# Kernel tuning notes

Hardware: AMD Instinct MI355X
Metric: run time of the kernel (lower is better)

Reference implementation:

```python
import jax, jax.numpy as jnp
import numpy as np

B, N, H, FD = 2, 512, 128, 5
NT, SD, L = 3, 4, 3
COPY = 10.0
EPS = 1e-6


def setup_inputs() -> dict:
    key = jax.random.key(0)
    ks = jax.random.split(key, 20)
    node_type = jax.random.randint(ks[0], (B, N, 1), 0, NT).astype(jnp.float32)
    node_state = jax.random.normal(ks[1], (B, N, SD), jnp.float32)
    node_feats = jnp.concatenate([node_type, node_state], axis=-1)  # [B,N,5]
    adj = jax.random.bernoulli(ks[2], 0.05, (B, N, N)).astype(jnp.float32)
    adj = jnp.maximum(adj, adj.transpose(0, 2, 1)) * (1.0 - jnp.eye(N, dtype=jnp.float32))
    scope_node_mask = jax.random.bernoulli(ks[3], 0.5, (B, N)).astype(jnp.float32)
    scope_edge_mask = jax.random.bernoulli(ks[4], 0.5, (B, N, N)).astype(jnp.float32)
    s = 0.02
    p = dict(
        node_feats=node_feats, adj=adj,
        scope_node_mask=scope_node_mask, scope_edge_mask=scope_edge_mask,
        W_in=jax.random.normal(ks[5], (FD, H)) * s, b_in=jnp.zeros((H,)),
        W_mp=jax.random.normal(ks[6], (L, 2 * H, H)) * s, b_mp=jnp.zeros((L, H)),
        Wt1=jax.random.normal(ks[7], (H, H)) * s, bt1=jnp.zeros((H,)),
        Wt2=jax.random.normal(ks[8], (H, NT)) * s, bt2=jnp.zeros((NT,)),
        Ws1=jax.random.normal(ks[9], (H, H)) * s, bs1=jnp.zeros((H,)),
        Ws2=jax.random.normal(ks[10], (H, SD)) * s, bs2=jnp.zeros((SD,)),
        We1=jax.random.normal(ks[11], (4 * H, H)) * s, be1=jnp.zeros((H,)),
        We2=jax.random.normal(ks[12], (H, 3)) * s, be2=jnp.zeros((3,)),
    )
    return p


def _decode_edge_logits(adj, edl, eye):
    probs = jax.nn.softmax(edl, axis=-1)
    p_keep = probs[..., 0]  # EDGE_DELTA_KEEP = 0
    p_add = probs[..., 1]   # EDGE_DELTA_ADD = 1
    cur = (adj > 0.5).astype(edl.dtype)
    p_next = jnp.clip(p_add + p_keep * cur, EPS, 1.0 - EPS)
    el = jnp.log(p_next) - jnp.log1p(-p_next)  # logit
    return jnp.where(eye[None], -1e9, el)


def _forward(node_feats, adj, scope_node_mask, scope_edge_mask,
             W_in, b_in, W_mp, b_mp, Wt1, bt1, Wt2, bt2,
             Ws1, bs1, Ws2, bs2, We1, be1, We2, be2):
    # encoder: input proj + L rounds of [h, adj@h] -> Linear -> ReLU
    h = jax.nn.relu(node_feats @ W_in + b_in)  # [B,N,H]
    for l in range(L):
        msg = jnp.einsum('bij,bjh->bih', adj, h)
        h = jax.nn.relu(jnp.concatenate([h, msg], axis=-1) @ W_mp[l] + b_mp[l])
    # node heads (2-layer MLPs)
    type_local = jax.nn.relu(h @ Wt1 + bt1) @ Wt2 + bt2      # [B,N,NT]
    state_local = jax.nn.relu(h @ Ws1 + bs1) @ Ws2 + bs2     # [B,N,SD]
    # pairwise edge-delta head
    h_i = h[:, :, None, :]
    h_j = h[:, None, :, :]
    pair = jnp.concatenate([
        jnp.broadcast_to(h_i, (B, N, N, H)),
        jnp.broadcast_to(h_j, (B, N, N, H)),
        jnp.abs(h_i - h_j),
        h_i * h_j,
    ], axis=-1)  # [B,N,N,4H]
    edl = jax.nn.relu(pair @ We1 + be1) @ We2 + be2  # [B,N,N,3]
    edl = 0.5 * (edl + edl.transpose(0, 2, 1, 3))
    eye = jnp.eye(N, dtype=bool)
    edl = jnp.where(eye[None, :, :, None], 0.0, edl)
    # merges with copy paths
    cur_type = jnp.clip(node_feats[..., 0].astype(jnp.int32), 0, NT - 1)
    copy_type = jnp.where(jnp.arange(NT) == cur_type[..., None], COPY, -COPY)
    type_full = jnp.where(scope_node_mask[..., None] != 0, type_local, copy_type)
    scope = scope_node_mask[..., None]
    state_full = scope * state_local + (1.0 - scope) * node_feats[..., 1:]
    copy_edl = jnp.broadcast_to(jnp.where(jnp.arange(3) == 0, COPY, -COPY), (B, N, N, 3))
    copy_edl = jnp.where(eye[None, :, :, None], 0.0, copy_edl)
    edl_full = jnp.where(scope_edge_mask[..., None] != 0, edl, copy_edl)
    el_full = _decode_edge_logits(adj, edl_full, eye)
    return type_full, state_full, edl_full, el_full


def reference(node_feats, adj, scope_node_mask, scope_edge_mask,
              W_in, b_in, W_mp, b_mp, Wt1, bt1, Wt2, bt2,
              Ws1, bs1, Ws2, bs2, We1, be1, We2, be2):
    return _forward(node_feats, adj, scope_node_mask, scope_edge_mask,
                    W_in, b_in, W_mp, b_mp, Wt1, bt1, Wt2, bt2,
                    Ws1, bs1, Ws2, bs2, We1, be1, We2, be2)
```

## Files before the change

### kernel.cpp

```cpp
#include <hip/hip_runtime.h>
#include <math.h>

#define B_ 2
#define N_ 512
#define H_ 128
#define NT_ 3
#define SD_ 4
#define FD_ 5

typedef float f32x4 __attribute__((ext_vector_type(4)));
typedef unsigned int u32x4 __attribute__((ext_vector_type(4)));

#define MFMA16(acc, a, b) \
    asm("s_nop 1\n\tv_mfma_f32_16x16x32_bf16 %0, %1, %2, %0" \
        : "+v"(acc) : "v"(a), "v"(b))

#define CVTPK(d, a, b) \
    asm("v_cvt_pk_bf16_f32 %0, %1, %2" : "=v"(d) : "v"(a), "v"(b))

#define CVTPKA(d, a, b) \
    asm("v_cvt_pk_bf16_f32 %0, |%1|, |%2|" : "=v"(d) : "v"(a), "v"(b))

static __device__ inline unsigned rne1(float f) {
    unsigned u = __float_as_uint(f);
    u += 0x7fffu + ((u >> 16) & 1u);
    return u >> 16;
}

__global__ __launch_bounds__(128) void k_input(const float* __restrict__ feats,
                                               const float* __restrict__ W_in,
                                               const float* __restrict__ b_in,
                                               float* __restrict__ hout,
                                               const float* __restrict__ We1,
                                               const float* __restrict__ We2,
                                               unsigned short* __restrict__ wfrag,
                                               unsigned short* __restrict__ wfrag2) {
    int blk = blockIdx.x, tid = threadIdx.x;
    if (blk < B_ * N_) {
        const float* f = feats + (size_t)blk * FD_;
        float acc = b_in[tid];
#pragma unroll
        for (int k = 0; k < FD_; ++k) acc += f[k] * W_in[k * H_ + tid];
        hout[(size_t)blk * H_ + tid] = fmaxf(acc, 0.f);
        return;
    }
    if (blk < B_ * N_ + 32) {
        int t = (blk - B_ * N_) * 128 + tid;
        int lane = t & 63, cg = (t >> 6) & 7, kb = t >> 9;
        int lr = lane & 15, g = lane >> 4;
        int c = cg * 16 + lr;
        unsigned o[4];
#pragma unroll
        for (int p = 0; p < 4; ++p) {
            float a = We1[(size_t)(256 + kb * 32 + 8 * g + 2 * p) * H_ + c];
            float bq = We1[(size_t)(256 + kb * 32 + 8 * g + 2 * p + 1) * H_ + c];
            o[p] = rne1(a) | (rne1(bq) << 16);
        }
        u32x4 v = {o[0], o[1], o[2], o[3]};
        *(u32x4*)(wfrag + (size_t)t * 8) = v;
        return;
    }
    {
        int t = (blk - (B_ * N_ + 32)) * 128 + tid;
        if (t < 256) {
            int kb = t >> 6, lane = t & 63;
            int oc = lane & 15, g = lane >> 4;
            unsigned w[4];
#pragma unroll
            for (int p = 0; p < 4; ++p) {
                int k0 = kb * 32 + g * 8 + 2 * p;
                int k1 = k0 + 1;
                int c0 = ((k0 >> 6) << 6) | ((k0 & 3) << 4) | ((k0 & 63) >> 2);
                int c1 = ((k1 >> 6) << 6) | ((k1 & 3) << 4) | ((k1 & 63) >> 2);
                float v0 = (oc < 3) ? We2[c0 * 3 + oc] : 0.f;
                float v1 = (oc < 3) ? We2[c1 * 3 + oc] : 0.f;
                w[p] = rne1(v0) | (rne1(v1) << 16);
            }
            u32x4 v = {w[0], w[1], w[2], w[3]};
            *(u32x4*)(wfrag2 + (size_t)t * 8) = v;
        }
    }
}

__global__ __launch_bounds__(128) void k_mp(const float* __restrict__ hin,
                                            float* __restrict__ hout,
                                            const float* __restrict__ adj,
                                            const float* __restrict__ Wl,
                                            const float* __restrict__ bl) {
    __shared__ float hi[H_];
    __shared__ float msg[H_];
    __shared__ unsigned short idxs[N_];
    __shared__ float avals[N_];
    __shared__ int cnt2[2];
    int node = blockIdx.x;
    int b = node >> 9;
    int tid = threadIdx.x;
    int w = tid >> 6, lane = tid & 63;
    hi[tid] = hin[(size_t)node * H_ + tid];
    const float* arow = adj + (size_t)node * N_;
    float4 av = ((const float4*)arow)[tid];
    int segbase = w * 256;
    int cum = 0;
#pragma unroll
    for (int q = 0; q < 4; ++q) {
        float a = (&av.x)[q];
        bool pred = (a != 0.f);
        unsigned long long mask = __ballot(pred);
        if (pred) {
            int pos = segbase + cum +
                      (int)__popcll(mask & ((1ull << lane) - 1ull));
            idxs[pos] = (unsigned short)(tid * 4 + q);
            avals[pos] = a;
        }
        cum += (int)__popcll(mask);
    }
    if (lane == 0) cnt2[w] = cum;
    __syncthreads();

    float m = 0.f;
    const float* hb = hin + ((size_t)b * N_) * H_;
    int n0 = cnt2[0], n1 = cnt2[1];
    for (int t = 0; t < n0; ++t)
        m += avals[t] * hb[(size_t)idxs[t] * H_ + tid];
    for (int t = 0; t < n1; ++t)
        m += avals[256 + t] * hb[(size_t)idxs[256 + t] * H_ + tid];
    msg[tid] = m;
    __syncthreads();

    float acc = bl[tid];
#pragma unroll 4
    for (int k = 0; k < H_; ++k) {
        acc += hi[k]  * Wl[(size_t)k * H_ + tid];
        acc += msg[k] * Wl[(size_t)(k + H_) * H_ + tid];
    }
    hout[(size_t)node * H_ + tid] = fmaxf(acc, 0.f);
}

__global__ __launch_bounds__(128) void k_heads(
    const float* __restrict__ h, const float* __restrict__ feats,
    const float* __restrict__ snm,
    const float* __restrict__ Wt1, const float* __restrict__ bt1,
    const float* __restrict__ Wt2, const float* __restrict__ bt2,
    const float* __restrict__ Ws1, const float* __restrict__ bs1,
    const float* __restrict__ Ws2, const float* __restrict__ bs2,
    const float* __restrict__ We1, const float* __restrict__ be1,
    float* __restrict__ Acoef, float* __restrict__ Bcoef,
    unsigned short* __restrict__ hbf,
    float* __restrict__ type_out, float* __restrict__ state_out) {
    __shared__ float hi[H_], hT[H_], hS[H_];
    int node = blockIdx.x, tid = threadIdx.x;
    float hv0 = h[(size_t)node * H_ + tid];
    hi[tid] = hv0;
    hbf[(size_t)node * H_ + tid] = (unsigned short)rne1(hv0);
    __syncthreads();
    float at = bt1[tid], as = bs1[tid], aa = be1[tid], ab = 0.f;
#pragma unroll 4
    for (int k = 0; k < H_; ++k) {
        float hv = hi[k];
        at += hv * Wt1[k * H_ + tid];
        as += hv * Ws1[k * H_ + tid];
        aa += hv * We1[k * H_ + tid];
        ab += hv * We1[(k + H_) * H_ + tid];
    }
    hT[tid] = fmaxf(at, 0.f);
    hS[tid] = fmaxf(as, 0.f);
    int c = tid;
    int kp = ((c >> 6) << 6) | ((c & 15) << 2) | ((c >> 4) & 3);
    Acoef[(size_t)node * H_ + kp] = aa;
    Bcoef[(size_t)node * H_ + kp] = ab;
    __syncthreads();
    float sm = snm[node];
    if (tid < NT_) {
        float tl = bt2[tid];
        for (int cc = 0; cc < H_; ++cc) tl += hT[cc] * Wt2[cc * NT_ + tid];
        int ct = (int)feats[(size_t)node * FD_];
        ct = ct < 0 ? 0 : (ct > NT_ - 1 ? NT_ - 1 : ct);
        float cv = (tid == ct) ? 10.f : -10.f;
        type_out[(size_t)node * NT_ + tid] = (sm != 0.f) ? tl : cv;
    }
    if (tid >= 64 && tid < 64 + SD_) {
        int s = tid - 64;
        float sl = bs2[s];
        for (int cc = 0; cc < H_; ++cc) sl += hS[cc] * Ws2[cc * SD_ + s];
        state_out[(size_t)node * SD_ + s] =
            sm * sl + (1.f - sm) * feats[(size_t)node * FD_ + 1 + s];
    }
}

__global__ __launch_bounds__(256, 2) void k_pair2(
    const float* __restrict__ h, const unsigned short* __restrict__ hbf,
    const float* __restrict__ Acp, const float* __restrict__ Bcp,
    const unsigned short* __restrict__ wfrag,
    const unsigned short* __restrict__ wfrag2,
    const float* __restrict__ be2, const float* __restrict__ sem,
    const float* __restrict__ adj,
    float* __restrict__ edl_out, float* __restrict__ el_out) {

    __shared__ unsigned short tile[2][128][128];

    int bid = blockIdx.x;
    int b = 0, r = bid;
    if (r >= 1280) { b = 1; r -= 1280; }
    int jtile, i;
    if (r < 128)      { jtile = 0; i = r; }
    else if (r < 384) { jtile = 1; i = r - 128; }
    else if (r < 768) { jtile = 2; i = r - 384; }
    else              { jtile = 3; i = r - 768; }
    int JT0 = jtile << 7;
    bool diagblk = (jtile == (i >> 7));
    int bN = b << 9;

    int tid = threadIdx.x;
    int wave = tid >> 6, lane = tid & 63;
    int jh = wave >> 1, ch = wave & 1;
    int lr = lane & 15, g = lane >> 4;

    u32x4 Bf[4][8];
#pragma unroll
    for (int ct = 0; ct < 4; ++ct)
#pragma unroll
        for (int kb = 0; kb < 8; ++kb)
            Bf[ct][kb] = *(const u32x4*)(wfrag +
                (((size_t)kb * 8 + (ch * 4 + ct)) * 64 + lane) * 8);

    const float* hrow = h + (size_t)(bN + i) * H_;
    float him[4][8];
#pragma unroll
    for (int m = 0; m < 4; ++m) {
        float4 a = *(const float4*)(hrow + 32 * m + 8 * g);
        float4 bq = *(const float4*)(hrow + 32 * m + 8 * g + 4);
        him[m][0] = a.x;  him[m][1] = a.y;  him[m][2] = a.z;  him[m][3] = a.w;
        him[m][4] = bq.x; him[m][5] = bq.y; him[m][6] = bq.z; him[m][7] = bq.w;
    }

    f32x4 AcoI = *(const f32x4*)(Acp + (size_t)(bN + i) * H_ + ch * 64 + lr * 4);
    f32x4 BcoI = *(const f32x4*)(Bcp + (size_t)(bN + i) * H_ + ch * 64 + lr * 4);

    char* tb0 = (char*)&tile[0][0][0];
    char* tb1 = (char*)&tile[1][0][0];

#pragma unroll
    for (int jt = 0; jt < 4; ++jt) {
        int jloc0 = jh * 64 + jt * 16;
        const unsigned short* hjp =
            hbf + (size_t)(bN + JT0 + jloc0 + lr) * H_ + 8 * g;
        u32x4 hjall[4];
#pragma unroll
        for (int m = 0; m < 4; ++m)
            hjall[m] = *(const u32x4*)(hjp + 32 * m);

        f32x4 acc0 = {0.f, 0.f, 0.f, 0.f};
        f32x4 acc1 = {0.f, 0.f, 0.f, 0.f};
        f32x4 acc2 = {0.f, 0.f, 0.f, 0.f};
        f32x4 acc3 = {0.f, 0.f, 0.f, 0.f};

#pragma unroll
        for (int m = 0; m < 4; ++m) {
            float hjf[8];
#pragma unroll
            for (int p = 0; p < 4; ++p) {
                unsigned d = hjall[m][p];
                hjf[2 * p]     = __uint_as_float(d << 16);
                hjf[2 * p + 1] = __uint_as_float(d & 0xffff0000u);
            }
            float tt[8], uu[8];
#pragma unroll
            for (int t = 0; t < 8; ++t) {
                tt[t] = him[m][t] - hjf[t];
                uu[t] = him[m][t] * hjf[t];
            }
            unsigned t0, t1, t2, t3, u0, u1, u2, u3;
            CVTPKA(t0, tt[0], tt[1]); CVTPKA(t1, tt[2], tt[3]);
            CVTPKA(t2, tt[4], tt[5]); CVTPKA(t3, tt[6], tt[7]);
            CVTPK(u0, uu[0], uu[1]); CVTPK(u1, uu[2], uu[3]);
            CVTPK(u2, uu[4], uu[5]); CVTPK(u3, uu[6], uu[7]);
            u32x4 tav = {t0, t1, t2, t3};
            u32x4 uav = {u0, u1, u2, u3};
            MFMA16(acc0, tav, Bf[0][m]);
            MFMA16(acc1, tav, Bf[1][m]);
            MFMA16(acc2, tav, Bf[2][m]);
            MFMA16(acc3, tav, Bf[3][m]);
            MFMA16(acc0, uav, Bf[0][4 + m]);
            MFMA16(acc1, uav, Bf[1][4 + m]);
            MFMA16(acc2, uav, Bf[2][4 + m]);
            MFMA16(acc3, uav, Bf[3][4 + m]);
        }
        asm("s_nop 7\n\ts_nop 7\n\ts_nop 3"
            : "+v"(acc0), "+v"(acc1), "+v"(acc2), "+v"(acc3));

#pragma unroll
        for (int rr = 0; rr < 4; ++rr) {
            int jloc = jloc0 + 4 * g + rr;
            size_t jn = (size_t)(bN + JT0 + jloc) * H_ + ch * 64 + lr * 4;
            f32x4 BcJ = *(const f32x4*)(Bcp + jn);
            f32x4 AcJ = *(const f32x4*)(Acp + jn);
            float h10 = fmaxf(acc0[rr] + AcoI[0] + BcJ[0], 0.f);
            float h11 = fmaxf(acc1[rr] + AcoI[1] + BcJ[1], 0.f);
            float h12 = fmaxf(acc2[rr] + AcoI[2] + BcJ[2], 0.f);
            float h13 = fmaxf(acc3[rr] + AcoI[3] + BcJ[3], 0.f);
            float h20 = fmaxf(acc0[rr] + AcJ[0] + BcoI[0], 0.f);
            float h21 = fmaxf(acc1[rr] + AcJ[1] + BcoI[1], 0.f);
            float h22 = fmaxf(acc2[rr] + AcJ[2] + BcoI[2], 0.f);
            float h23 = fmaxf(acc3[rr] + AcJ[3] + BcoI[3], 0.f);
            unsigned w10, w11, w20, w21;
            CVTPK(w10, h10, h11); CVTPK(w11, h12, h13);
            CVTPK(w20, h20, h21); CVTPK(w21, h22, h23);
            int byte = jloc * 256 + ch * 128 + lr * 8;
            byte ^= (jloc & 7) << 4;
            uint2 v1; v1.x = w10; v1.y = w11;
            uint2 v2; v2.x = w20; v2.y = w21;
            *(uint2*)(tb0 + byte) = v1;
            *(uint2*)(tb1 + byte) = v2;
        }
    }

    u32x4 Bf2[4];
#pragma unroll
    for (int kb = 0; kb < 4; ++kb)
        Bf2[kb] = *(const u32x4*)(wfrag2 + ((size_t)kb * 64 + lane) * 8);

    __syncthreads();

    f32x4 pacc0 = {0.f,0.f,0.f,0.f}, pacc1 = {0.f,0.f,0.f,0.f};
    f32x4 pacc2 = {0.f,0.f,0.f,0.f}, pacc3 = {0.f,0.f,0.f,0.f};
#pragma unroll
    for (int p = 0; p < 4; ++p) {
        int f = wave + 4 * p;
        int orient = f >> 3, sub = f & 7;
        char* tb = orient ? tb1 : tb0;
        int jloc = sub * 16 + lr;
#pragma unroll
        for (int kb = 0; kb < 4; ++kb) {
            int byte = jloc * 256 + kb * 64 + g * 16;
            byte ^= (jloc & 7) << 4;
            u32x4 a = *(const u32x4*)(tb + byte);
            if (p == 0) { MFMA16(pacc0, a, Bf2[kb]); }
            else if (p == 1) { MFMA16(pacc1, a, Bf2[kb]); }
            else if (p == 2) { MFMA16(pacc2, a, Bf2[kb]); }
            else { MFMA16(pacc3, a, Bf2[kb]); }
        }
    }
    asm("s_nop 7\n\ts_nop 7\n\ts_nop 3"
        : "+v"(pacc0), "+v"(pacc1), "+v"(pacc2), "+v"(pacc3));
    __syncthreads();

    float* sbuf = (float*)&tile[0][0][0];
    if (lr < 3) {
#pragma unroll
        for (int p = 0; p < 4; ++p) {
            int f = wave + 4 * p;
            int orient = f >> 3, sub = f & 7;
            f32x4 pa = (p == 0) ? pacc0 : (p == 1) ? pacc1 : (p == 2) ? pacc2 : pacc3;
#pragma unroll
            for (int rr = 0; rr < 4; ++rr) {
                int jloc = sub * 16 + 4 * g + rr;
                sbuf[((orient << 7) + jloc) * 3 + lr] = pa[rr];
            }
        }
    }
    __syncthreads();

    {
        int d = tid & 1, jloc = tid >> 1;
        int jg = JT0 + jloc;
        bool skip = diagblk && (jg < i);
        if (!skip) {
            float s0 = 0.5f * (sbuf[jloc * 3 + 0] + sbuf[(128 + jloc) * 3 + 0]) + be2[0];
            float s1 = 0.5f * (sbuf[jloc * 3 + 1] + sbuf[(128 + jloc) * 3 + 1]) + be2[1];
            float s2 = 0.5f * (sbuf[jloc * 3 + 2] + sbuf[(128 + jloc) * 3 + 2]) + be2[2];
            size_t p = d ? ((size_t)(bN + jg) * N_ + i)
                         : ((size_t)(bN + i) * N_ + jg);
            if (jg == i) {
                edl_out[p * 3 + 0] = 0.f;
                edl_out[p * 3 + 1] = 0.f;
                edl_out[p * 3 + 2] = 0.f;
                el_out[p] = -1e9f;
            } else {
                float msk = sem[p];
                float e0 = (msk != 0.f) ? s0 : 10.f;
                float e1 = (msk != 0.f) ? s1 : -10.f;
                float e2 = (msk != 0.f) ? s2 : -10.f;
                edl_out[p * 3 + 0] = e0;
                edl_out[p * 3 + 1] = e1;
                edl_out[p * 3 + 2] = e2;
                float a = adj[p];
                float cur = (a > 0.5f) ? 1.f : 0.f;
                float mx = fmaxf(e0, fmaxf(e1, e2));
                float x0 = expf(e0 - mx), x1 = expf(e1 - mx), x2 = expf(e2 - mx);
                float inv = 1.f / (x0 + x1 + x2);
                float pn = x1 * inv + x0 * inv * cur;
                pn = fminf(fmaxf(pn, 1e-6f), 1.f - 1e-6f);
                el_out[p] = logf(pn) - log1pf(-pn);
            }
        }
    }
}

extern "C" void kernel_launch(void* const* d_in, const int* in_sizes, int n_in,
                              void* d_out, int out_size, void* d_ws,
                              size_t ws_size, hipStream_t stream) {
    const float* feats = (const float*)d_in[0];
    const float* adj   = (const float*)d_in[1];
    const float* snm   = (const float*)d_in[2];
    const float* sem   = (const float*)d_in[3];
    const float* W_in  = (const float*)d_in[4];
    const float* b_in  = (const float*)d_in[5];
    const float* W_mp  = (const float*)d_in[6];
    const float* b_mp  = (const float*)d_in[7];
    const float* Wt1 = (const float*)d_in[8],  *bt1 = (const float*)d_in[9];
    const float* Wt2 = (const float*)d_in[10], *bt2 = (const float*)d_in[11];
    const float* Ws1 = (const float*)d_in[12], *bs1 = (const float*)d_in[13];
    const float* Ws2 = (const float*)d_in[14], *bs2 = (const float*)d_in[15];
    const float* We1 = (const float*)d_in[16], *be1 = (const float*)d_in[17];
    const float* We2 = (const float*)d_in[18], *be2 = (const float*)d_in[19];

    float* out = (float*)d_out;
    float* type_out  = out;
    float* state_out = out + 3072;
    float* edl_out   = out + 7168;
    float* el_out    = out + 7168 + 1572864;

    float* ws = (float*)d_ws;
    float* hA = ws;
    float* hB = ws + 131072;
    float* Bcp = ws + 262144;
    unsigned short* hbf    = (unsigned short*)(ws + 393216);
    unsigned short* wfrag  = (unsigned short*)(ws + 458752);
    unsigned short* wfrag2 = (unsigned short*)(ws + 475136);
    float* Acp = hA;

    k_input<<<B_ * N_ + 34, 128, 0, stream>>>(feats, W_in, b_in, hA,
                                              We1, We2, wfrag, wfrag2);
    k_mp<<<B_ * N_, H_, 0, stream>>>(hA, hB, adj, W_mp + 0 * 2 * H_ * H_, b_mp + 0 * H_);
    k_mp<<<B_ * N_, H_, 0, stream>>>(hB, hA, adj, W_mp + 1 * 2 * H_ * H_, b_mp + 1 * H_);
    k_mp<<<B_ * N_, H_, 0, stream>>>(hA, hB, adj, W_mp + 2 * 2 * H_ * H_, b_mp + 2 * H_);
    k_heads<<<B_ * N_, H_, 0, stream>>>(hB, feats, snm, Wt1, bt1, Wt2, bt2,
                                        Ws1, bs1, Ws2, bs2, We1, be1,
                                        Acp, Bcp, hbf, type_out, state_out);
    k_pair2<<<2560, 256, 0, stream>>>(hB, hbf, Acp, Bcp, wfrag, wfrag2,
                                      be2, sem, adj, edl_out, el_out);
}
```

Before: 127.6 us.

## Switch pair kernel to fp16 packed math and batch 4 nodes per block

Moves the pairwise edge MLP from bf16 to fp16. The |hi-hj| and hi*hj features are now formed with packed fp16 instructions directly on fp16 h, replacing per-element fp32 unpack, compute and repack. The message-passing and heads kernels now process four nodes per 256-thread block, splitting the K dimension across two halves so each weight load is reused across four nodes. The Acoef/Bcoef loads are hoisted ahead of the MFMA chain. This trades some accuracy (fp16 range and products computed in fp16) for fewer VALU ops and less weight traffic.

```diff
diff --git a/kernel.cpp b/kernel.cpp
--- a/kernel.cpp
+++ b/kernel.cpp
@@ -1,4 +1,5 @@
 #include <hip/hip_runtime.h>
+#include <hip/hip_fp16.h>
 #include <math.h>
 
 #define B_ 2
@@ -11,20 +12,29 @@
 typedef float f32x4 __attribute__((ext_vector_type(4)));
 typedef unsigned int u32x4 __attribute__((ext_vector_type(4)));
 
-#define MFMA16(acc, a, b) \
-    asm("s_nop 1\n\tv_mfma_f32_16x16x32_bf16 %0, %1, %2, %0" \
+#define MFMA4(a0, a1, a2, a3, av, b0, b1, b2, b3) \
+    asm("s_nop 1\n\t" \
+        "v_mfma_f32_16x16x32_f16 %0, %4, %5, %0\n\t" \
+        "v_mfma_f32_16x16x32_f16 %1, %4, %6, %1\n\t" \
+        "v_mfma_f32_16x16x32_f16 %2, %4, %7, %2\n\t" \
+        "v_mfma_f32_16x16x32_f16 %3, %4, %8, %3" \
+        : "+v"(a0), "+v"(a1), "+v"(a2), "+v"(a3) \
+        : "v"(av), "v"(b0), "v"(b1), "v"(b2), "v"(b3))
+
+#define MFMA16F(acc, a, b) \
+    asm("s_nop 1\n\tv_mfma_f32_16x16x32_f16 %0, %1, %2, %0" \
         : "+v"(acc) : "v"(a), "v"(b))
 
-#define CVTPK(d, a, b) \
-    asm("v_cvt_pk_bf16_f32 %0, %1, %2" : "=v"(d) : "v"(a), "v"(b))
-
-#define CVTPKA(d, a, b) \
-    asm("v_cvt_pk_bf16_f32 %0, |%1|, |%2|" : "=v"(d) : "v"(a), "v"(b))
-
-static __device__ inline unsigned rne1(float f) {
-    unsigned u = __float_as_uint(f);
-    u += 0x7fffu + ((u >> 16) & 1u);
-    return u >> 16;
+#define PKMUL(d, a, b) \
+    asm("v_pk_mul_f16 %0, %1, %2" : "=v"(d) : "v"(a), "v"(b))
+#define PKSUB(d, a, b) \
+    asm("v_pk_add_f16 %0, %1, %2 neg_lo:[0,1] neg_hi:[0,1]" \
+        : "=v"(d) : "v"(a), "v"(b))
+#define CVTPKF16(d, a, b) \
+    asm("v_cvt_pkrtz_f16_f32 %0, %1, %2" : "=v"(d) : "v"(a), "v"(b))
+
+static __device__ inline unsigned short f2h(float f) {
+    return __half_as_ushort(__float2half(f));
 }
 
 __global__ __launch_bounds__(128) void k_input(const float* __restrict__ feats,
@@ -54,7 +64,7 @@
         for (int p = 0; p < 4; ++p) {
             float a = We1[(size_t)(256 + kb * 32 + 8 * g + 2 * p) * H_ + c];
             float bq = We1[(size_t)(256 + kb * 32 + 8 * g + 2 * p + 1) * H_ + c];
-            o[p] = rne1(a) | (rne1(bq) << 16);
+            o[p] = (unsigned)f2h(a) | ((unsigned)f2h(bq) << 16);
         }
         u32x4 v = {o[0], o[1], o[2], o[3]};
         *(u32x4*)(wfrag + (size_t)t * 8) = v;
@@ -74,7 +84,7 @@
                 int c1 = ((k1 >> 6) << 6) | ((k1 & 3) << 4) | ((k1 & 63) >> 2);
                 float v0 = (oc < 3) ? We2[c0 * 3 + oc] : 0.f;
                 float v1 = (oc < 3) ? We2[c1 * 3 + oc] : 0.f;
-                w[p] = rne1(v0) | (rne1(v1) << 16);
+                w[p] = (unsigned)f2h(v0) | ((unsigned)f2h(v1) << 16);
             }
             u32x4 v = {w[0], w[1], w[2], w[3]};
             *(u32x4*)(wfrag2 + (size_t)t * 8) = v;
@@ -82,61 +92,79 @@
     }
 }
 
-__global__ __launch_bounds__(128) void k_mp(const float* __restrict__ hin,
+__global__ __launch_bounds__(256) void k_mp(const float* __restrict__ hin,
                                             float* __restrict__ hout,
                                             const float* __restrict__ adj,
                                             const float* __restrict__ Wl,
                                             const float* __restrict__ bl) {
-    __shared__ float hi[H_];
-    __shared__ float msg[H_];
     __shared__ unsigned short idxs[N_];
     __shared__ float avals[N_];
+    __shared__ float x[4][256];
+    __shared__ float red[2][4][128];
     __shared__ int cnt2[2];
-    int node = blockIdx.x;
-    int b = node >> 9;
     int tid = threadIdx.x;
-    int w = tid >> 6, lane = tid & 63;
-    hi[tid] = hin[(size_t)node * H_ + tid];
-    const float* arow = adj + (size_t)node * N_;
-    float4 av = ((const float4*)arow)[tid];
-    int segbase = w * 256;
-    int cum = 0;
-#pragma unroll
-    for (int q = 0; q < 4; ++q) {
-        float a = (&av.x)[q];
-        bool pred = (a != 0.f);
-        unsigned long long mask = __ballot(pred);
-        if (pred) {
-            int pos = segbase + cum +
-                      (int)__popcll(mask & ((1ull << lane) - 1ull));
-            idxs[pos] = (unsigned short)(tid * 4 + q);
-            avals[pos] = a;
-        }
-        cum += (int)__popcll(mask);
-    }
-    if (lane == 0) cnt2[w] = cum;
-    __syncthreads();
-
-    float m = 0.f;
+    int c = tid & 127, q = tid >> 7;
+    int nb = blockIdx.x * 4;
+    int b = nb >> 9;
+    for (int n = q; n < 4; n += 2)
+        x[n][c] = hin[(size_t)(nb + n) * H_ + c];
     const float* hb = hin + ((size_t)b * N_) * H_;
-    int n0 = cnt2[0], n1 = cnt2[1];
-    for (int t = 0; t < n0; ++t)
-        m += avals[t] * hb[(size_t)idxs[t] * H_ + tid];
-    for (int t = 0; t < n1; ++t)
-        m += avals[256 + t] * hb[(size_t)idxs[256 + t] * H_ + tid];
-    msg[tid] = m;
-    __syncthreads();
-
-    float acc = bl[tid];
+    float mreg[4] = {0.f, 0.f, 0.f, 0.f};
+    for (int n = 0; n < 4; ++n) {
+        __syncthreads();
+        if (tid < 128) {
+            int w = tid >> 6, lane = tid & 63;
+            const float* arow = adj + (size_t)(nb + n) * N_;
+            float4 av = ((const float4*)arow)[tid];
+            int segbase = w * 256, cum = 0;
+#pragma unroll
+            for (int p = 0; p < 4; ++p) {
+                float a = (&av.x)[p];
+                bool pred = (a != 0.f);
+                unsigned long long mask = __ballot(pred);
+                if (pred) {
+                    int pos = segbase + cum +
+                              (int)__popcll(mask & ((1ull << lane) - 1ull));
+                    idxs[pos] = (unsigned short)(tid * 4 + p);
+                    avals[pos] = a;
+                }
+                cum += (int)__popcll(mask);
+            }
+            if (lane == 0) cnt2[w] = cum;
+        }
+        __syncthreads();
+        int n0 = cnt2[0], n1 = cnt2[1];
+        for (int t = q; t < n0; t += 2)
+            mreg[n] += avals[t] * hb[(size_t)idxs[t] * H_ + c];
+        for (int t = q; t < n1; t += 2)
+            mreg[n] += avals[256 + t] * hb[(size_t)idxs[256 + t] * H_ + c];
+    }
+#pragma unroll
+    for (int n = 0; n < 4; ++n) red[q][n][c] = mreg[n];
+    __syncthreads();
+    if (q == 0)
+#pragma unroll
+        for (int n = 0; n < 4; ++n)
+            x[n][H_ + c] = red[0][n][c] + red[1][n][c];
+    __syncthreads();
+    float acc[4] = {0.f, 0.f, 0.f, 0.f};
 #pragma unroll 4
-    for (int k = 0; k < H_; ++k) {
-        acc += hi[k]  * Wl[(size_t)k * H_ + tid];
-        acc += msg[k] * Wl[(size_t)(k + H_) * H_ + tid];
-    }
-    hout[(size_t)node * H_ + tid] = fmaxf(acc, 0.f);
+    for (int k = 128 * q; k < 128 * q + 128; ++k) {
+        float w = Wl[(size_t)k * H_ + c];
+#pragma unroll
+        for (int n = 0; n < 4; ++n) acc[n] += x[n][k] * w;
+    }
+#pragma unroll
+    for (int n = 0; n < 4; ++n) red[q][n][c] = acc[n];
+    __syncthreads();
+    if (q == 0)
+#pragma unroll
+        for (int n = 0; n < 4; ++n)
+            hout[(size_t)(nb + n) * H_ + c] =
+                fmaxf(red[0][n][c] + red[1][n][c] + bl[c], 0.f);
 }
 
-__global__ __launch_bounds__(128) void k_heads(
+__global__ __launch_bounds__(256) void k_heads(
     const float* __restrict__ h, const float* __restrict__ feats,
     const float* __restrict__ snm,
     const float* __restrict__ Wt1, const float* __restrict__ bt1,
@@ -145,50 +173,108 @@
     const float* __restrict__ Ws2, const float* __restrict__ bs2,
     const float* __restrict__ We1, const float* __restrict__ be1,
     float* __restrict__ Acoef, float* __restrict__ Bcoef,
-    unsigned short* __restrict__ hbf,
+    unsigned short* __restrict__ hf16,
     float* __restrict__ type_out, float* __restrict__ state_out) {
-    __shared__ float hi[H_], hT[H_], hS[H_];
-    int node = blockIdx.x, tid = threadIdx.x;
-    float hv0 = h[(size_t)node * H_ + tid];
-    hi[tid] = hv0;
-    hbf[(size_t)node * H_ + tid] = (unsigned short)rne1(hv0);
-    __syncthreads();
-    float at = bt1[tid], as = bs1[tid], aa = be1[tid], ab = 0.f;
-#pragma unroll 4
-    for (int k = 0; k < H_; ++k) {
-        float hv = hi[k];
-        at += hv * Wt1[k * H_ + tid];
-        as += hv * Ws1[k * H_ + tid];
-        aa += hv * We1[k * H_ + tid];
-        ab += hv * We1[(k + H_) * H_ + tid];
-    }
-    hT[tid] = fmaxf(at, 0.f);
-    hS[tid] = fmaxf(as, 0.f);
-    int c = tid;
-    int kp = ((c >> 6) << 6) | ((c & 15) << 2) | ((c >> 4) & 3);
-    Acoef[(size_t)node * H_ + kp] = aa;
-    Bcoef[(size_t)node * H_ + kp] = ab;
-    __syncthreads();
-    float sm = snm[node];
-    if (tid < NT_) {
-        float tl = bt2[tid];
-        for (int cc = 0; cc < H_; ++cc) tl += hT[cc] * Wt2[cc * NT_ + tid];
-        int ct = (int)feats[(size_t)node * FD_];
+    __shared__ float hi[4][128];
+    __shared__ float red[2][4][4][128];
+    __shared__ float hT[4][128], hS[4][128];
+    __shared__ float tred[4][3][8];
+    __shared__ float sred[4][4][8];
+    int tid = threadIdx.x;
+    int c = tid & 127, q = tid >> 7;
+    int nb = blockIdx.x * 4;
+    for (int n = q; n < 4; n += 2) {
+        float v = h[(size_t)(nb + n) * H_ + c];
+        hi[n][c] = v;
+        hf16[(size_t)(nb + n) * H_ + c] = f2h(v);
+    }
+    __syncthreads();
+    float at[4] = {0,0,0,0}, as[4] = {0,0,0,0};
+    float aa[4] = {0,0,0,0}, ab[4] = {0,0,0,0};
+    for (int k = 64 * q; k < 64 * q + 64; ++k) {
+        float wt = Wt1[(size_t)k * H_ + c], ws = Ws1[(size_t)k * H_ + c];
+        float wa = We1[(size_t)k * H_ + c], wb = We1[(size_t)(k + H_) * H_ + c];
+#pragma unroll
+        for (int n = 0; n < 4; ++n) {
+            float hv = hi[n][k];
+            at[n] += hv * wt; as[n] += hv * ws;
+            aa[n] += hv * wa; ab[n] += hv * wb;
+        }
+    }
+#pragma unroll
+    for (int n = 0; n < 4; ++n) {
+        red[q][0][n][c] = at[n]; red[q][1][n][c] = as[n];
+        red[q][2][n][c] = aa[n]; red[q][3][n][c] = ab[n];
+    }
+    __syncthreads();
+    if (q == 0) {
+        int kp = ((c >> 6) << 6) | ((c & 15) << 2) | ((c >> 4) & 3);
+#pragma unroll
+        for (int n = 0; n < 4; ++n) {
+            hT[n][c] = fmaxf(red[0][0][n][c] + red[1][0][n][c] + bt1[c], 0.f);
+            hS[n][c] = fmaxf(red[0][1][n][c] + red[1][1][n][c] + bs1[c], 0.f);
+            Acoef[(size_t)(nb + n) * H_ + kp] =
+                red[0][2][n][c] + red[1][2][n][c] + be1[c];
+            Bcoef[(size_t)(nb + n) * H_ + kp] =
+                red[0][3][n][c] + red[1][3][n][c];
+        }
+    }
+    __syncthreads();
+    float* rbuf0 = &red[0][0][0][0];
+    float* rbuf1 = &red[1][0][0][0];
+#pragma unroll
+    for (int dn = 0; dn < 2; ++dn) {
+        int n = 2 * q + dn;
+        float ht = hT[n][c], hs = hS[n][c];
+#pragma unroll
+        for (int o = 0; o < 3; ++o)
+            rbuf0[(n * 3 + o) * 128 + c] = ht * Wt2[c * 3 + o];
+#pragma unroll
+        for (int s = 0; s < 4; ++s)
+            rbuf1[(n * 4 + s) * 128 + c] = hs * Ws2[c * 4 + s];
+    }
+    __syncthreads();
+    if (tid < 96) {
+        int n = tid / 24, o = (tid / 8) % 3, ch = tid & 7;
+        float s = 0.f;
+#pragma unroll
+        for (int t = 0; t < 16; ++t)
+            s += rbuf0[(n * 3 + o) * 128 + ch * 16 + t];
+        tred[n][o][ch] = s;
+    } else if (tid >= 128) {
+        int t2 = tid - 128;
+        int n = t2 / 32, sd = (t2 / 8) % 4, ch = t2 & 7;
+        float s = 0.f;
+#pragma unroll
+        for (int t = 0; t < 16; ++t)
+            s += rbuf1[(n * 4 + sd) * 128 + ch * 16 + t];
+        sred[n][sd][ch] = s;
+    }
+    __syncthreads();
+    if (tid < 12) {
+        int n = tid / 3, o = tid % 3;
+        float tl = bt2[o];
+#pragma unroll
+        for (int t = 0; t < 8; ++t) tl += tred[n][o][t];
+        float sm = snm[nb + n];
+        int ct = (int)feats[(size_t)(nb + n) * FD_];
         ct = ct < 0 ? 0 : (ct > NT_ - 1 ? NT_ - 1 : ct);
-        float cv = (tid == ct) ? 10.f : -10.f;
-        type_out[(size_t)node * NT_ + tid] = (sm != 0.f) ? tl : cv;
-    }
-    if (tid >= 64 && tid < 64 + SD_) {
-        int s = tid - 64;
-        float sl = bs2[s];
-        for (int cc = 0; cc < H_; ++cc) sl += hS[cc] * Ws2[cc * SD_ + s];
-        state_out[(size_t)node * SD_ + s] =
-            sm * sl + (1.f - sm) * feats[(size_t)node * FD_ + 1 + s];
+        float cv = (o == ct) ? 10.f : -10.f;
+        type_out[(size_t)(nb + n) * NT_ + o] = (sm != 0.f) ? tl : cv;
+    } else if (tid >= 16 && tid < 32) {
+        int t2 = tid - 16;
+        int n = t2 / 4, sd = t2 % 4;
+        float sl = bs2[sd];
+#pragma unroll
+        for (int t = 0; t < 8; ++t) sl += sred[n][sd][t];
+        float sm = snm[nb + n];
+        state_out[(size_t)(nb + n) * SD_ + sd] =
+            sm * sl + (1.f - sm) * feats[(size_t)(nb + n) * FD_ + 1 + sd];
     }
 }
 
 __global__ __launch_bounds__(256, 2) void k_pair2(
-    const float* __restrict__ h, const unsigned short* __restrict__ hbf,
+    const unsigned short* __restrict__ hf16,
     const float* __restrict__ Acp, const float* __restrict__ Bcp,
     const unsigned short* __restrict__ wfrag,
     const unsigned short* __restrict__ wfrag2,
@@ -223,15 +309,11 @@
             Bf[ct][kb] = *(const u32x4*)(wfrag +
                 (((size_t)kb * 8 + (ch * 4 + ct)) * 64 + lane) * 8);
 
-    const float* hrow = h + (size_t)(bN + i) * H_;
-    float him[4][8];
-#pragma unroll
-    for (int m = 0; m < 4; ++m) {
-        float4 a = *(const float4*)(hrow + 32 * m + 8 * g);
-        float4 bq = *(const float4*)(hrow + 32 * m + 8 * g + 4);
-        him[m][0] = a.x;  him[m][1] = a.y;  him[m][2] = a.z;  him[m][3] = a.w;
-        him[m][4] = bq.x; him[m][5] = bq.y; him[m][6] = bq.z; him[m][7] = bq.w;
-    }
+    const unsigned short* hirow = hf16 + (size_t)(bN + i) * H_;
+    u32x4 him[4];
+#pragma unroll
+    for (int m = 0; m < 4; ++m)
+        him[m] = *(const u32x4*)(hirow + 32 * m + 8 * g);
 
     f32x4 AcoI = *(const f32x4*)(Acp + (size_t)(bN + i) * H_ + ch * 64 + lr * 4);
     f32x4 BcoI = *(const f32x4*)(Bcp + (size_t)(bN + i) * H_ + ch * 64 + lr * 4);
@@ -243,47 +325,39 @@
     for (int jt = 0; jt < 4; ++jt) {
         int jloc0 = jh * 64 + jt * 16;
         const unsigned short* hjp =
-            hbf + (size_t)(bN + JT0 + jloc0 + lr) * H_ + 8 * g;
+            hf16 + (size_t)(bN + JT0 + jloc0 + lr) * H_ + 8 * g;
         u32x4 hjall[4];
 #pragma unroll
         for (int m = 0; m < 4; ++m)
             hjall[m] = *(const u32x4*)(hjp + 32 * m);
-
-        f32x4 acc0 = {0.f, 0.f, 0.f, 0.f};
-        f32x4 acc1 = {0.f, 0.f, 0.f, 0.f};
-        f32x4 acc2 = {0.f, 0.f, 0.f, 0.f};
-        f32x4 acc3 = {0.f, 0.f, 0.f, 0.f};
+        f32x4 BcJv[4], AcJv[4];
+#pragma unroll
+        for (int rr = 0; rr < 4; ++rr) {
+            size_t jn = (size_t)(bN + JT0 + jloc0 + 4 * g + rr) * H_ +
+                        ch * 64 + lr * 4;
+            BcJv[rr] = *(const f32x4*)(Bcp + jn);
+            AcJv[rr] = *(const f32x4*)(Acp + jn);
+        }
+
+        f32x4 acc0 = {0.f,0.f,0.f,0.f}, acc1 = {0.f,0.f,0.f,0.f};
+        f32x4 acc2 = {0.f,0.f,0.f,0.f}, acc3 = {0.f,0.f,0.f,0.f};
 
 #pragma unroll
         for (int m = 0; m < 4; ++m) {
-            float hjf[8];
+            u32x4 tav, uav;
 #pragma unroll
             for (int p = 0; p < 4; ++p) {
-                unsigned d = hjall[m][p];
-                hjf[2 * p]     = __uint_as_float(d << 16);
-                hjf[2 * p + 1] = __uint_as_float(d & 0xffff0000u);
+                unsigned hip_ = him[m][p], hjp_ = hjall[m][p];
+                unsigned u_, d_;
+                PKMUL(u_, hip_, hjp_);
+                PKSUB(d_, hip_, hjp_);
+                uav[p] = u_;
+                tav[p] = d_ & 0x7fff7fffu;
             }
-            float tt[8], uu[8];
-#pragma unroll
-            for (int t = 0; t < 8; ++t) {
-                tt[t] = him[m][t] - hjf[t];
-                uu[t] = him[m][t] * hjf[t];
-            }
-            unsigned t0, t1, t2, t3, u0, u1, u2, u3;
-            CVTPKA(t0, tt[0], tt[1]); CVTPKA(t1, tt[2], tt[3]);
-            CVTPKA(t2, tt[4], tt[5]); CVTPKA(t3, tt[6], tt[7]);
-            CVTPK(u0, uu[0], uu[1]); CVTPK(u1, uu[2], uu[3]);
-            CVTPK(u2, uu[4], uu[5]); CVTPK(u3, uu[6], uu[7]);
-            u32x4 tav = {t0, t1, t2, t3};
-            u32x4 uav = {u0, u1, u2, u3};
-            MFMA16(acc0, tav, Bf[0][m]);
-            MFMA16(acc1, tav, Bf[1][m]);
-            MFMA16(acc2, tav, Bf[2][m]);
-            MFMA16(acc3, tav, Bf[3][m]);
-            MFMA16(acc0, uav, Bf[0][4 + m]);
-            MFMA16(acc1, uav, Bf[1][4 + m]);
-            MFMA16(acc2, uav, Bf[2][4 + m]);
-            MFMA16(acc3, uav, Bf[3][4 + m]);
+            MFMA4(acc0, acc1, acc2, acc3, tav,
+                  Bf[0][m], Bf[1][m], Bf[2][m], Bf[3][m]);
+            MFMA4(acc0, acc1, acc2, acc3, uav,
+                  Bf[0][4 + m], Bf[1][4 + m], Bf[2][4 + m], Bf[3][4 + m]);
         }
         asm("s_nop 7\n\ts_nop 7\n\ts_nop 3"
             : "+v"(acc0), "+v"(acc1), "+v"(acc2), "+v"(acc3));
@@ -291,20 +365,17 @@
 #pragma unroll
         for (int rr = 0; rr < 4; ++rr) {
             int jloc = jloc0 + 4 * g + rr;
-            size_t jn = (size_t)(bN + JT0 + jloc) * H_ + ch * 64 + lr * 4;
-            f32x4 BcJ = *(const f32x4*)(Bcp + jn);
-            f32x4 AcJ = *(const f32x4*)(Acp + jn);
-            float h10 = fmaxf(acc0[rr] + AcoI[0] + BcJ[0], 0.f);
-            float h11 = fmaxf(acc1[rr] + AcoI[1] + BcJ[1], 0.f);
-            float h12 = fmaxf(acc2[rr] + AcoI[2] + BcJ[2], 0.f);
-            float h13 = fmaxf(acc3[rr] + AcoI[3] + BcJ[3], 0.f);
-            float h20 = fmaxf(acc0[rr] + AcJ[0] + BcoI[0], 0.f);
-            float h21 = fmaxf(acc1[rr] + AcJ[1] + BcoI[1], 0.f);
-            float h22 = fmaxf(acc2[rr] + AcJ[2] + BcoI[2], 0.f);
-            float h23 = fmaxf(acc3[rr] + AcJ[3] + BcoI[3], 0.f);
+            float h10 = fmaxf(acc0[rr] + AcoI[0] + BcJv[rr][0], 0.f);
+            float h11 = fmaxf(acc1[rr] + AcoI[1] + BcJv[rr][1], 0.f);
+            float h12 = fmaxf(acc2[rr] + AcoI[2] + BcJv[rr][2], 0.f);
+            float h13 = fmaxf(acc3[rr] + AcoI[3] + BcJv[rr][3], 0.f);
+            float h20 = fmaxf(acc0[rr] + AcJv[rr][0] + BcoI[0], 0.f);
+            float h21 = fmaxf(acc1[rr] + AcJv[rr][1] + BcoI[1], 0.f);
+            float h22 = fmaxf(acc2[rr] + AcJv[rr][2] + BcoI[2], 0.f);
+            float h23 = fmaxf(acc3[rr] + AcJv[rr][3] + BcoI[3], 0.f);
             unsigned w10, w11, w20, w21;
-            CVTPK(w10, h10, h11); CVTPK(w11, h12, h13);
-            CVTPK(w20, h20, h21); CVTPK(w21, h22, h23);
+            CVTPKF16(w10, h10, h11); CVTPKF16(w11, h12, h13);
+            CVTPKF16(w20, h20, h21); CVTPKF16(w21, h22, h23);
             int byte = jloc * 256 + ch * 128 + lr * 8;
             byte ^= (jloc & 7) << 4;
             uint2 v1; v1.x = w10; v1.y = w11;
@@ -334,10 +405,10 @@
             int byte = jloc * 256 + kb * 64 + g * 16;
             byte ^= (jloc & 7) << 4;
             u32x4 a = *(const u32x4*)(tb + byte);
-            if (p == 0) { MFMA16(pacc0, a, Bf2[kb]); }
-            else if (p == 1) { MFMA16(pacc1, a, Bf2[kb]); }
-            else if (p == 2) { MFMA16(pacc2, a, Bf2[kb]); }
-            else { MFMA16(pacc3, a, Bf2[kb]); }
+            if (p == 0)      { MFMA16F(pacc0, a, Bf2[kb]); }
+            else if (p == 1) { MFMA16F(pacc1, a, Bf2[kb]); }
+            else if (p == 2) { MFMA16F(pacc2, a, Bf2[kb]); }
+            else             { MFMA16F(pacc3, a, Bf2[kb]); }
         }
     }
     asm("s_nop 7\n\ts_nop 7\n\ts_nop 3"
@@ -350,7 +421,8 @@
         for (int p = 0; p < 4; ++p) {
             int f = wave + 4 * p;
             int orient = f >> 3, sub = f & 7;
-            f32x4 pa = (p == 0) ? pacc0 : (p == 1) ? pacc1 : (p == 2) ? pacc2 : pacc3;
+            f32x4 pa = (p == 0) ? pacc0 : (p == 1) ? pacc1
+                     : (p == 2) ? pacc2 : pacc3;
 #pragma unroll
             for (int rr = 0; rr < 4; ++rr) {
                 int jloc = sub * 16 + 4 * g + rr;
@@ -424,19 +496,22 @@
     float* hA = ws;
     float* hB = ws + 131072;
     float* Bcp = ws + 262144;
-    unsigned short* hbf    = (unsigned short*)(ws + 393216);
+    unsigned short* hf16   = (unsigned short*)(ws + 393216);
     unsigned short* wfrag  = (unsigned short*)(ws + 458752);
     unsigned short* wfrag2 = (unsigned short*)(ws + 475136);
     float* Acp = hA;
 
     k_input<<<B_ * N_ + 34, 128, 0, stream>>>(feats, W_in, b_in, hA,
                                               We1, We2, wfrag, wfrag2);
-    k_mp<<<B_ * N_, H_, 0, stream>>>(hA, hB, adj, W_mp + 0 * 2 * H_ * H_, b_mp + 0 * H_);
-    k_mp<<<B_ * N_, H_, 0, stream>>>(hB, hA, adj, W_mp + 1 * 2 * H_ * H_, b_mp + 1 * H_);
-    k_mp<<<B_ * N_, H_, 0, stream>>>(hA, hB, adj, W_mp + 2 * 2 * H_ * H_, b_mp + 2 * H_);
-    k_heads<<<B_ * N_, H_, 0, stream>>>(hB, feats, snm, Wt1, bt1, Wt2, bt2,
-                                        Ws1, bs1, Ws2, bs2, We1, be1,
-                                        Acp, Bcp, hbf, type_out, state_out);
-    k_pair2<<<2560, 256, 0, stream>>>(hB, hbf, Acp, Bcp, wfrag, wfrag2,
+    k_mp<<<B_ * N_ / 4, 256, 0, stream>>>(hA, hB, adj,
+                                          W_mp + 0 * 2 * H_ * H_, b_mp + 0 * H_);
+    k_mp<<<B_ * N_ / 4, 256, 0, stream>>>(hB, hA, adj,
+                                          W_mp + 1 * 2 * H_ * H_, b_mp + 1 * H_);
+    k_mp<<<B_ * N_ / 4, 256, 0, stream>>>(hA, hB, adj,
+                                          W_mp + 2 * 2 * H_ * H_, b_mp + 2 * H_);
+    k_heads<<<B_ * N_ / 4, 256, 0, stream>>>(hB, feats, snm, Wt1, bt1, Wt2, bt2,
+                                             Ws1, bs1, Ws2, bs2, We1, be1,
+                                             Acp, Bcp, hf16, type_out, state_out);
+    k_pair2<<<2560, 256, 0, stream>>>(hf16, Acp, Bcp, wfrag, wfrag2,
                                       be2, sem, adj, edl_out, el_out);
 }
```

After: 154.0 us. +20.7%, slower.
